# Performance work log

Measured on AMD Instinct MI355X. Metric: run time of the kernel, lower is better.

Reference implementation:

```python
import jax, jax.numpy as jnp
import numpy as np


def setup_inputs() -> dict:
    key = jax.random.key(0)
    k1, k2 = jax.random.split(key)
    N, K, C = 2, 32, 32
    h, w = 64, 64
    H, W = 1024, 1024
    grid = jax.random.normal(k1, (N, K, C, h, w), dtype=jnp.float32)
    guidemap = jax.random.normal(k2, (N, C, H, W), dtype=jnp.float32)
    return {"grid": grid, "guidemap": guidemap}


def reference(grid, guidemap):
    N, C, H, W = guidemap.shape
    h, w = grid.shape[3], grid.shape[4]
    f1, f2 = H // h, W // w
    # F.unfold with kernel==stride (non-overlapping blocks):
    # [N,C,H,W] -> [N,C,f1*f2,h,w] with kernel elements row-major within a block.
    g = guidemap.reshape(N, C, h, f1, w, f2)
    g = g.transpose(0, 1, 3, 5, 2, 4).reshape(N, C, f1 * f2, h, w)
    # Per-location small contraction over channels C.
    out = jnp.einsum('ikjmn,ijlmn->iklmn', grid, g)  # [N,K,f1*f2,h,w]
    # F.fold with kernel==stride (non-overlapping scatter, no overlap-add):
    out = out.reshape(N, -1, f1, f2, h, w)
    out = out.transpose(0, 1, 4, 2, 5, 3).reshape(N, -1, H, W)
    return out
```

## Files before the change

kernel.cpp:

```cpp
#include <hip/hip_runtime.h>


namespace {
constexpr int K = 32, C = 32;
constexpr int W = 1024;
constexpr int HW = 1024 * 1024;
constexpr size_t GRDN = (size_t)K * C * 64 * 64;
}

typedef float v4f __attribute__((ext_vector_type(4)));

__device__ __forceinline__ void gl_lds4(const float* src, float* dst) {
    __builtin_amdgcn_global_load_lds(
        (const __attribute__((address_space(1))) void*)src,
        (__attribute__((address_space(3))) void*)dst, 4, 0, 0);
}

__global__ __launch_bounds__(256, 4) void gridup_kernel(
    const float* __restrict__ grd,
    const float* __restrict__ gm,
    float* __restrict__ out)
{
    __shared__ float sM[2][C][K];

    const int b  = blockIdx.x;
    const int wp = (b & 7) * 512 + (b >> 3);
    const int t  = threadIdx.x;

    const int g0  = wp * 2;
    const int n   = g0 >> 12;
    const int rr  = g0 & 4095;
    const int by  = rr >> 6;
    const int bx0 = rr & 63;

    #pragma unroll
    for (int i = 0; i < 8; ++i) {
        const int e  = i * 256 + t;
        const int tl = e >> 10;
        const int c  = (e >> 5) & 31;
        const int k  = e & 31;
        gl_lds4(grd + (size_t)n * GRDN + (size_t)(k * 32 + c) * 4096 +
                    by * 64 + bx0 + tl,
                &sM[0][0][0] + e);
    }
    __syncthreads();

    const int w  = t >> 6;
    const int tl = w >> 1;
    const int kh = w & 1;
    const int l  = t & 63;
    const int bx = bx0 + tl;

    const int row = l >> 2;
    const int col = (l & 3) << 2;
    const size_t pix = (size_t)(by * 16 + row) * W + bx * 16 + col;
    const float* gb = gm + (size_t)n * C * HW + pix;
    float*       ob = out + ((size_t)n * K + kh * 16) * HW + pix;
    const float* Mb = &sM[tl][0][kh * 16];

    v4f g[4];
    #pragma unroll
    for (int j = 0; j < 4; ++j)
        g[j] = *reinterpret_cast<const v4f*>(gb + (size_t)j * HW);

    v4f acc[16];
    #pragma unroll
    for (int k = 0; k < 16; ++k) acc[k] = (v4f)0.f;

    #pragma unroll
    for (int c = 0; c < C; ++c) {
        const v4f u = g[c & 3];
        if (c + 4 < C)
            g[c & 3] = *reinterpret_cast<const v4f*>(gb + (size_t)(c + 4) * HW);
        #pragma unroll
        for (int kq = 0; kq < 4; ++kq) {
            const v4f m = *reinterpret_cast<const v4f*>(Mb + c * K + kq * 4);
            acc[kq * 4 + 0] += m.x * u;
            acc[kq * 4 + 1] += m.y * u;
            acc[kq * 4 + 2] += m.z * u;
            acc[kq * 4 + 3] += m.w * u;
        }
    }

    #pragma unroll
    for (int k = 0; k < 16; ++k) {
        *reinterpret_cast<v4f*>(ob + (size_t)k * HW) = acc[k];
    }
}

extern "C" void kernel_launch(void* const* d_in, const int* in_sizes, int n_in,
                              void* d_out, int out_size, void* d_ws, size_t ws_size,
                              hipStream_t stream) {
    const float* grd = (const float*)d_in[0];
    const float* gm  = (const float*)d_in[1];
    float* out = (float*)d_out;

    gridup_kernel<<<4096, 256, 0, stream>>>(grd, gm, out);
}
```

Measured before the change: 167.4 us.

## Map one grid cell per block with 2-pixel threads and all-channel prefetch

Each block now handles a single 16x16 grid cell instead of two, so the block count doubles and each thread computes 2 pixels by 16 output channels instead of 4. All 32 guidemap channel loads are issued up front rather than through a 4-deep rolling prefetch. The goal is more memory-level parallelism and more blocks in flight for this bandwidth-bound kernel. The cost is narrower 8-byte global loads and stores and the same LDS matrix reads amortized over half as many pixels.

```diff
diff --git a/kernel.cpp b/kernel.cpp
--- a/kernel.cpp
+++ b/kernel.cpp
@@ -8,6 +8,7 @@
 constexpr size_t GRDN = (size_t)K * C * 64 * 64;
 }
 
+typedef float v2f __attribute__((ext_vector_type(2)));
 typedef float v4f __attribute__((ext_vector_type(4)));
 
 __device__ __forceinline__ void gl_lds4(const float* src, float* dst) {
@@ -21,57 +22,53 @@
     const float* __restrict__ gm,
     float* __restrict__ out)
 {
-    __shared__ float sM[2][C][K];
+    __shared__ float sM[C][K];
 
     const int b  = blockIdx.x;
-    const int wp = (b & 7) * 512 + (b >> 3);
+    const int gt = (b & 7) * 1024 + (b >> 3);
     const int t  = threadIdx.x;
 
-    const int g0  = wp * 2;
-    const int n   = g0 >> 12;
-    const int rr  = g0 & 4095;
-    const int by  = rr >> 6;
-    const int bx0 = rr & 63;
+    const int n  = gt >> 12;
+    const int rr = gt & 4095;
+    const int by = rr >> 6;
+    const int bx = rr & 63;
 
     #pragma unroll
-    for (int i = 0; i < 8; ++i) {
-        const int e  = i * 256 + t;
-        const int tl = e >> 10;
-        const int c  = (e >> 5) & 31;
-        const int k  = e & 31;
+    for (int i = 0; i < 4; ++i) {
+        const int e = i * 256 + t;
+        const int c = e >> 5;
+        const int k = e & 31;
         gl_lds4(grd + (size_t)n * GRDN + (size_t)(k * 32 + c) * 4096 +
-                    by * 64 + bx0 + tl,
-                &sM[0][0][0] + e);
+                    by * 64 + bx,
+                &sM[0][0] + e);
     }
     __syncthreads();
 
     const int w  = t >> 6;
-    const int tl = w >> 1;
-    const int kh = w & 1;
+    const int ph = w & 1;
+    const int kh = w >> 1;
     const int l  = t & 63;
-    const int bx = bx0 + tl;
 
-    const int row = l >> 2;
-    const int col = (l & 3) << 2;
+    const int p   = ph * 128 + l * 2;
+    const int row = p >> 4;
+    const int col = p & 15;
     const size_t pix = (size_t)(by * 16 + row) * W + bx * 16 + col;
     const float* gb = gm + (size_t)n * C * HW + pix;
     float*       ob = out + ((size_t)n * K + kh * 16) * HW + pix;
-    const float* Mb = &sM[tl][0][kh * 16];
+    const float* Mb = &sM[0][kh * 16];
 
-    v4f g[4];
+    v2f g[32];
     #pragma unroll
-    for (int j = 0; j < 4; ++j)
-        g[j] = *reinterpret_cast<const v4f*>(gb + (size_t)j * HW);
+    for (int c = 0; c < C; ++c)
+        g[c] = *reinterpret_cast<const v2f*>(gb + (size_t)c * HW);
 
-    v4f acc[16];
+    v2f acc[16];
     #pragma unroll
-    for (int k = 0; k < 16; ++k) acc[k] = (v4f)0.f;
+    for (int k = 0; k < 16; ++k) acc[k] = (v2f)0.f;
 
     #pragma unroll
     for (int c = 0; c < C; ++c) {
-        const v4f u = g[c & 3];
-        if (c + 4 < C)
-            g[c & 3] = *reinterpret_cast<const v4f*>(gb + (size_t)(c + 4) * HW);
+        const v2f u = g[c];
         #pragma unroll
         for (int kq = 0; kq < 4; ++kq) {
             const v4f m = *reinterpret_cast<const v4f*>(Mb + c * K + kq * 4);
@@ -84,7 +81,7 @@
 
     #pragma unroll
     for (int k = 0; k < 16; ++k) {
-        *reinterpret_cast<v4f*>(ob + (size_t)k * HW) = acc[k];
+        *reinterpret_cast<v2f*>(ob + (size_t)k * HW) = acc[k];
     }
 }
 
@@ -95,5 +92,5 @@
     const float* gm  = (const float*)d_in[1];
     float* out = (float*)d_out;
 
-    gridup_kernel<<<4096, 256, 0, stream>>>(grd, gm, out);
+    gridup_kernel<<<8192, 256, 0, stream>>>(grd, gm, out);
 }
```

After: 185.4 us. 10.8% more time.
